# Optimization experiments

Measured on AMD Instinct MI355X. Metric: run time of the kernel, lower is better.

The kernel has to match this reference:

```python
import jax, jax.numpy as jnp
import numpy as np

# Faithful math of CustomAttn(method='tanh').forward:
#   E[i,j] = Linear_{4h->1}( tanh( concat(e_i, e_j) ) )
#          = w[:2h] . tanh(e_i) + w[2h:] . tanh(e_j) + b
#   out    = softmax(E, axis=0)
# Since tanh is elementwise and the linear layer is a dot product, the
# pairwise score decomposes into a_i + b_j + bias, computed with two
# O(n*d) matvecs and one broadcasted add (honoring the original math
# exactly while avoiding the O(n^2) python loop).

SEQ_LEN = 8192
HIDDEN = 256  # hidden_size; feature dim of encoder_outputs is 2*HIDDEN


def setup_inputs() -> dict:
    key = jax.random.key(0)
    k1, k2 = jax.random.split(key)
    encoder_outputs = jax.random.normal(k1, (SEQ_LEN, 2 * HIDDEN), dtype=jnp.float32)
    attn2_w = jax.random.normal(k2, (4 * HIDDEN,), dtype=jnp.float32) * (1.0 / np.sqrt(4 * HIDDEN))
    attn2_b = jnp.zeros((1,), dtype=jnp.float32)
    return {"encoder_outputs": encoder_outputs, "attn2_w": attn2_w, "attn2_b": attn2_b}


def reference(encoder_outputs, attn2_w, attn2_b):
    d = encoder_outputs.shape[1]  # 2*hidden_size
    t = jnp.tanh(encoder_outputs)            # [S, 2h]
    a = t @ attn2_w[:d]                      # [S], contribution of e_i
    b = t @ attn2_w[d:]                      # [S], contribution of e_j
    energies = a[:, None] + b[None, :] + attn2_b[0]  # [S, S]
    return jax.nn.softmax(energies, axis=0)
```

## Files before the change

kernel.cpp:

```cpp
#include <hip/hip_runtime.h>
#include <math.h>

#define SEQ 8192
#define DIM 512

typedef float floatx4 __attribute__((ext_vector_type(4)));

__global__ __launch_bounds__(256) void ca_exp_a(
    const float* __restrict__ e, const float* __restrict__ w,
    float* __restrict__ exp_a) {
    const int wave = threadIdx.x >> 6;
    const int lane = threadIdx.x & 63;
    const int row  = blockIdx.x * 4 + wave;
    const float* er = e + (size_t)row * DIM + lane * 8;
    const float* wr = w + lane * 8;

    float4 e0 = *reinterpret_cast<const float4*>(er);
    float4 e1 = *reinterpret_cast<const float4*>(er + 4);
    float4 w0 = *reinterpret_cast<const float4*>(wr);
    float4 w1 = *reinterpret_cast<const float4*>(wr + 4);

    float sum = tanhf(e0.x) * w0.x + tanhf(e0.y) * w0.y +
                tanhf(e0.z) * w0.z + tanhf(e0.w) * w0.w +
                tanhf(e1.x) * w1.x + tanhf(e1.y) * w1.y +
                tanhf(e1.z) * w1.z + tanhf(e1.w) * w1.w;

    #pragma unroll
    for (int off = 32; off; off >>= 1) sum += __shfl_down(sum, off, 64);
    if (lane == 0) exp_a[row] = expf(sum);
}

__global__ __launch_bounds__(1024) void ca_norm_bcast(
    const float* __restrict__ exp_a, floatx4* __restrict__ out) {
    __shared__ float red[16];
    const int tid = threadIdx.x;

    const floatx4* ev = reinterpret_cast<const floatx4*>(exp_a);
    floatx4 v0 = ev[tid * 2];
    floatx4 v1 = ev[tid * 2 + 1];
    float s = ((v0.x + v0.y) + (v0.z + v0.w)) +
              ((v1.x + v1.y) + (v1.z + v1.w));
    #pragma unroll
    for (int off = 32; off; off >>= 1) s += __shfl_down(s, off, 64);
    if ((tid & 63) == 0) red[tid >> 6] = s;
    __syncthreads();
    float S = 0.f;
    #pragma unroll
    for (int i = 0; i < 16; ++i) S += red[i];
    const float inv = 1.0f / S;

    const int sub = tid >> 8;
    const int t   = tid & 255;
    const int row = blockIdx.x * 4 + sub;
    const float p = exp_a[row] * inv;
    floatx4 f;
    f.x = p; f.y = p; f.z = p; f.w = p;
    floatx4* o = out + (size_t)row * (SEQ / 4) + t;
    #pragma unroll
    for (int k = 0; k < 8; ++k)
        __builtin_nontemporal_store(f, o + k * 256);
}

extern "C" void kernel_launch(void* const* d_in, const int* in_sizes, int n_in,
                              void* d_out, int out_size, void* d_ws, size_t ws_size,
                              hipStream_t stream) {
    const float* enc = (const float*)d_in[0];
    const float* w   = (const float*)d_in[1];
    float* out = (float*)d_out;

    float* exp_a = (float*)d_ws;

    ca_exp_a<<<SEQ / 4, 256, 0, stream>>>(enc, w, exp_a);
    ca_norm_bcast<<<SEQ / 4, 1024, 0, stream>>>(exp_a, (floatx4*)out);
}
```

Baseline: 60.10 us.

## Split normalization into single-block kernel and separate broadcast kernel

```diff
diff --git a/kernel.cpp b/kernel.cpp
--- a/kernel.cpp
+++ b/kernel.cpp
@@ -30,11 +30,10 @@
     if (lane == 0) exp_a[row] = expf(sum);
 }
 
-__global__ __launch_bounds__(1024) void ca_norm_bcast(
-    const float* __restrict__ exp_a, floatx4* __restrict__ out) {
+__global__ __launch_bounds__(1024) void ca_normalize(
+    const float* __restrict__ exp_a, float* __restrict__ p) {
     __shared__ float red[16];
     const int tid = threadIdx.x;
-
     const floatx4* ev = reinterpret_cast<const floatx4*>(exp_a);
     floatx4 v0 = ev[tid * 2];
     floatx4 v1 = ev[tid * 2 + 1];
@@ -48,17 +47,29 @@
     #pragma unroll
     for (int i = 0; i < 16; ++i) S += red[i];
     const float inv = 1.0f / S;
+    floatx4 o0, o1;
+    o0.x = v0.x * inv; o0.y = v0.y * inv; o0.z = v0.z * inv; o0.w = v0.w * inv;
+    o1.x = v1.x * inv; o1.y = v1.y * inv; o1.z = v1.z * inv; o1.w = v1.w * inv;
+    floatx4* pv = reinterpret_cast<floatx4*>(p);
+    pv[tid * 2]     = o0;
+    pv[tid * 2 + 1] = o1;
+}
 
-    const int sub = tid >> 8;
-    const int t   = tid & 255;
-    const int row = blockIdx.x * 4 + sub;
-    const float p = exp_a[row] * inv;
-    floatx4 f;
-    f.x = p; f.y = p; f.z = p; f.w = p;
-    floatx4* o = out + (size_t)row * (SEQ / 4) + t;
+__global__ __launch_bounds__(256) void ca_bcast(
+    const float* __restrict__ p, floatx4* __restrict__ out) {
+    const int t = threadIdx.x;
+    const int rbase = blockIdx.x * 8;
+    float pv[8];
     #pragma unroll
-    for (int k = 0; k < 8; ++k)
-        __builtin_nontemporal_store(f, o + k * 256);
+    for (int r = 0; r < 8; ++r) pv[r] = p[rbase + r];
+    #pragma unroll
+    for (int r = 0; r < 8; ++r) {
+        floatx4 f;
+        f.x = pv[r]; f.y = pv[r]; f.z = pv[r]; f.w = pv[r];
+        floatx4* o = out + (size_t)(rbase + r) * (SEQ / 4) + t;
+        #pragma unroll
+        for (int k = 0; k < 8; ++k) o[k * 256] = f;
+    }
 }
 
 extern "C" void kernel_launch(void* const* d_in, const int* in_sizes, int n_in,
@@ -69,7 +80,9 @@
     float* out = (float*)d_out;
 
     float* exp_a = (float*)d_ws;
+    float* p     = exp_a + SEQ;
 
     ca_exp_a<<<SEQ / 4, 256, 0, stream>>>(enc, w, exp_a);
-    ca_norm_bcast<<<SEQ / 4, 1024, 0, stream>>>(exp_a, (floatx4*)out);
+    ca_normalize<<<1, 1024, 0, stream>>>(exp_a, p);
+    ca_bcast<<<SEQ / 8, 256, 0, stream>>>(p, (floatx4*)out);
 }
```

After: 55.86 us. 7.1% less time.

## Fuse exp and broadcast kernels into one cooperative kernel with grid sync

Applied to the files above, without the earlier changes.

```diff
diff --git a/kernel.cpp b/kernel.cpp
--- a/kernel.cpp
+++ b/kernel.cpp
@@ -1,64 +1,72 @@
 #include <hip/hip_runtime.h>
+#include <hip/hip_cooperative_groups.h>
 #include <math.h>
+
+namespace cg = cooperative_groups;
 
 #define SEQ 8192
 #define DIM 512
 
 typedef float floatx4 __attribute__((ext_vector_type(4)));
 
-__global__ __launch_bounds__(256) void ca_exp_a(
+__global__ __launch_bounds__(256) void ca_fused(
     const float* __restrict__ e, const float* __restrict__ w,
-    float* __restrict__ exp_a) {
-    const int wave = threadIdx.x >> 6;
-    const int lane = threadIdx.x & 63;
-    const int row  = blockIdx.x * 4 + wave;
-    const float* er = e + (size_t)row * DIM + lane * 8;
+    floatx4* __restrict__ out, float* __restrict__ partials) {
+    __shared__ float exps[8];
+    __shared__ float red[4];
+    __shared__ float S_sh;
+    const int tid  = threadIdx.x;
+    const int lane = tid & 63;
+    const int wv   = tid >> 6;
+    const int b    = blockIdx.x;
+
     const float* wr = w + lane * 8;
-
-    float4 e0 = *reinterpret_cast<const float4*>(er);
-    float4 e1 = *reinterpret_cast<const float4*>(er + 4);
-    float4 w0 = *reinterpret_cast<const float4*>(wr);
-    float4 w1 = *reinterpret_cast<const float4*>(wr + 4);
-
-    float sum = tanhf(e0.x) * w0.x + tanhf(e0.y) * w0.y +
-                tanhf(e0.z) * w0.z + tanhf(e0.w) * w0.w +
-                tanhf(e1.x) * w1.x + tanhf(e1.y) * w1.y +
-                tanhf(e1.z) * w1.z + tanhf(e1.w) * w1.w;
+    const float4 w0 = *reinterpret_cast<const float4*>(wr);
+    const float4 w1 = *reinterpret_cast<const float4*>(wr + 4);
 
     #pragma unroll
-    for (int off = 32; off; off >>= 1) sum += __shfl_down(sum, off, 64);
-    if (lane == 0) exp_a[row] = expf(sum);
-}
+    for (int rr = 0; rr < 2; ++rr) {
+        const int row = b * 8 + wv * 2 + rr;
+        const float* er = e + (size_t)row * DIM + lane * 8;
+        const float4 e0 = *reinterpret_cast<const float4*>(er);
+        const float4 e1 = *reinterpret_cast<const float4*>(er + 4);
+        float sum = tanhf(e0.x) * w0.x + tanhf(e0.y) * w0.y +
+                    tanhf(e0.z) * w0.z + tanhf(e0.w) * w0.w +
+                    tanhf(e1.x) * w1.x + tanhf(e1.y) * w1.y +
+                    tanhf(e1.z) * w1.z + tanhf(e1.w) * w1.w;
+        #pragma unroll
+        for (int off = 32; off; off >>= 1) sum += __shfl_down(sum, off, 64);
+        if (lane == 0) exps[wv * 2 + rr] = expf(sum);
+    }
+    __syncthreads();
+    if (tid == 0) {
+        float pa = 0.f;
+        #pragma unroll
+        for (int i = 0; i < 8; ++i) pa += exps[i];
+        partials[b] = pa;
+    }
 
-__global__ __launch_bounds__(1024) void ca_norm_bcast(
-    const float* __restrict__ exp_a, floatx4* __restrict__ out) {
-    __shared__ float red[16];
-    const int tid = threadIdx.x;
+    cg::this_grid().sync();
 
-    const floatx4* ev = reinterpret_cast<const floatx4*>(exp_a);
-    floatx4 v0 = ev[tid * 2];
-    floatx4 v1 = ev[tid * 2 + 1];
-    float s = ((v0.x + v0.y) + (v0.z + v0.w)) +
-              ((v1.x + v1.y) + (v1.z + v1.w));
+    const floatx4 pv = reinterpret_cast<const floatx4*>(partials)[tid];
+    float s = (pv.x + pv.y) + (pv.z + pv.w);
     #pragma unroll
     for (int off = 32; off; off >>= 1) s += __shfl_down(s, off, 64);
-    if ((tid & 63) == 0) red[tid >> 6] = s;
+    if (lane == 0) red[wv] = s;
     __syncthreads();
-    float S = 0.f;
+    if (tid == 0) S_sh = (red[0] + red[1]) + (red[2] + red[3]);
+    __syncthreads();
+    const float inv = 1.0f / S_sh;
+
     #pragma unroll
-    for (int i = 0; i < 16; ++i) S += red[i];
-    const float inv = 1.0f / S;
-
-    const int sub = tid >> 8;
-    const int t   = tid & 255;
-    const int row = blockIdx.x * 4 + sub;
-    const float p = exp_a[row] * inv;
-    floatx4 f;
-    f.x = p; f.y = p; f.z = p; f.w = p;
-    floatx4* o = out + (size_t)row * (SEQ / 4) + t;
-    #pragma unroll
-    for (int k = 0; k < 8; ++k)
-        __builtin_nontemporal_store(f, o + k * 256);
+    for (int r = 0; r < 8; ++r) {
+        const float p = exps[r] * inv;
+        floatx4 f;
+        f.x = p; f.y = p; f.z = p; f.w = p;
+        floatx4* o = out + (size_t)(b * 8 + r) * (SEQ / 4) + tid;
+        #pragma unroll
+        for (int k = 0; k < 8; ++k) o[k * 256] = f;
+    }
 }
 
 extern "C" void kernel_launch(void* const* d_in, const int* in_sizes, int n_in,
@@ -66,10 +74,10 @@
                               hipStream_t stream) {
     const float* enc = (const float*)d_in[0];
     const float* w   = (const float*)d_in[1];
-    float* out = (float*)d_out;
+    floatx4* out     = (floatx4*)d_out;
+    float* partials  = (float*)d_ws;
 
-    float* exp_a = (float*)d_ws;
-
-    ca_exp_a<<<SEQ / 4, 256, 0, stream>>>(enc, w, exp_a);
-    ca_norm_bcast<<<SEQ / 4, 1024, 0, stream>>>(exp_a, (floatx4*)out);
+    void* args[] = {(void*)&enc, (void*)&w, (void*)&out, (void*)&partials};
+    hipLaunchCooperativeKernel((const void*)ca_fused, dim3(1024), dim3(256),
+                               args, 0, stream);
 }
```

Result: slower. 102.5 us (+70.6%).
